# Optimization experiments

Measured on AMD Instinct MI355X. Metric: run time of the kernel, lower is better.

The kernel has to match this reference:

```python
import jax, jax.numpy as jnp
import numpy as np
from jax import lax

B, C, D, H, W = 4, 256, 32, 32, 32
LATENT = 512


def setup_inputs() -> dict:
    key = jax.random.key(0)
    k = jax.random.split(key, 6)
    x = jax.random.normal(k[0], (B, C, D, H, W), dtype=jnp.float32)
    prev_rgb = jax.random.normal(k[1], (B, 1, D, H, W), dtype=jnp.float32)
    istyle = jax.random.normal(k[2], (B, LATENT), dtype=jnp.float32)
    # nn.Linear(latent_dim, input_channel): weight [C, LATENT], bias [C]
    lim = 1.0 / np.sqrt(LATENT)
    W_style = jax.random.uniform(k[3], (C, LATENT), minval=-lim, maxval=lim, dtype=jnp.float32)
    b_style = jax.random.uniform(k[4], (C,), minval=-lim, maxval=lim, dtype=jnp.float32)
    # Conv3DMod weight [out=1, C, 1,1,1], kaiming_normal fan_in, leaky_relu(a=0) gain=sqrt(2)
    conv_weight = jax.random.normal(k[5], (1, C, 1, 1, 1), dtype=jnp.float32) * np.float32(np.sqrt(2.0 / C))
    return {"x": x, "prev_rgb": prev_rgb, "istyle": istyle,
            "W_style": W_style, "b_style": b_style, "conv_weight": conv_weight}


def _blur3d(x):
    # kornia filter3d with normalized 3x3x3 [1,2,1] outer-product kernel, replicate padding
    f = jnp.array([1.0, 2.0, 1.0], dtype=x.dtype)
    ker = f[:, None, None] * f[None, :, None] * f[None, None, :]
    ker = (ker / ker.sum())[None, None]  # [1,1,3,3,3] (single channel)
    xp = jnp.pad(x, ((0, 0), (0, 0), (1, 1), (1, 1), (1, 1)), mode='edge')
    return lax.conv_general_dilated(
        xp, ker, window_strides=(1, 1, 1), padding='VALID',
        dimension_numbers=('NCDHW', 'OIDHW', 'NCDHW'))


def reference(x, prev_rgb, istyle, W_style, b_style, conv_weight):
    b, c, d, h, w = x.shape
    # to_style linear
    style = istyle @ W_style.T + b_style                    # [b, c]
    # Conv3DMod, kernel=1, demod=False: per-sample modulated weights reduce to a
    # per-(sample, channel) coefficient; conv is a channel-weighted sum.
    wk = conv_weight[0, :, 0, 0, 0]                         # [c]
    coef = wk[None, :] * (style + 1.0)                      # [b, c]
    out = jnp.einsum('bcdhw,bc->bdhw', x, coef)[:, None]    # [b,1,d,h,w]
    out = out + prev_rgb
    # Upsample scale=2, trilinear, align_corners=False (half-pixel centers)
    out = jax.image.resize(out, (b, 1, 2 * d, 2 * h, 2 * w), method='trilinear')
    out = _blur3d(out)
    return out
```

## Files before the change

### kernel.cpp

```cpp
#include <hip/hip_runtime.h>

#define BATCH 4
#define CH    256
#define SVOL  32768
#define SV4   8192
#define NC    4
#define CCH   64


__global__ void __launch_bounds__(256)
coef_kernel(const float* __restrict__ istyle,
            const float* __restrict__ W_style,
            const float* __restrict__ b_style,
            const float* __restrict__ wk,
            float* __restrict__ coef) {
    int tid  = threadIdx.x;
    int wave = blockIdx.x * 4 + (tid >> 6);
    int lane = tid & 63;
    int b = wave >> 8;
    int c = wave & 255;
    const float* is = istyle + b * 512;
    const float* wr = W_style + c * 512;
    float acc = 0.f;
    #pragma unroll
    for (int j = 0; j < 8; ++j) {
        int k = lane + j * 64;
        acc += is[k] * wr[k];
    }
    #pragma unroll
    for (int off = 32; off >= 1; off >>= 1)
        acc += __shfl_down(acc, off, 64);
    if (lane == 0)
        coef[b * 256 + c] = wk[c] * (acc + b_style[c] + 1.0f);
}

__global__ void __launch_bounds__(256)
reduce_c_kernel(const float4* __restrict__ x4,
                const float* __restrict__ coef,
                float4* __restrict__ partial4) {
    __shared__ float cf[CCH];
    int chunk = blockIdx.y;
    int g  = blockIdx.x * 256 + threadIdx.x;
    int b  = g >> 13;
    int s4 = g & (SV4 - 1);
    if (threadIdx.x < CCH)
        cf[threadIdx.x] = coef[b * 256 + chunk * CCH + threadIdx.x];
    __syncthreads();
    const float4* xp = x4 + (size_t)(b * CH + chunk * CCH) * SV4 + s4;
    float4 acc = {0.f, 0.f, 0.f, 0.f};
    #pragma unroll 16
    for (int cc = 0; cc < CCH; ++cc) {
        float4 v = xp[(size_t)cc * SV4];
        float w = cf[cc];
        acc.x += v.x * w; acc.y += v.y * w;
        acc.z += v.z * w; acc.w += v.w * w;
    }
    partial4[(size_t)(chunk * BATCH + b) * SV4 + s4] = acc;
}

__global__ void __launch_bounds__(256)
finalize_small_kernel(const float4* __restrict__ partial4,
                      const float4* __restrict__ prev4,
                      float4* __restrict__ small4) {
    int g  = blockIdx.x * 256 + threadIdx.x;
    int b  = g >> 13;
    int s4 = g & (SV4 - 1);
    float4 acc = prev4[g];
    #pragma unroll
    for (int chunk = 0; chunk < NC; ++chunk) {
        float4 p = partial4[(size_t)(chunk * BATCH + b) * SV4 + s4];
        acc.x += p.x; acc.y += p.y; acc.z += p.z; acc.w += p.w;
    }
    small4[g] = acc;
}

__global__ void __launch_bounds__(256)
upblur_kernel(const float* __restrict__ small,
              float* __restrict__ out) {
    int g  = blockIdx.x * 256 + threadIdx.x;
    int xo = g & 63;
    int yo = (g >> 6) & 63;
    int zo = (g >> 12) & 63;
    int b  = g >> 18;

    int jx = xo >> 1, jy = yo >> 1, jz = zo >> 1;
    int px = xo & 1,  py = yo & 1,  pz = zo & 1;

    int xi[3] = { jx > 0 ? jx - 1 : 0, jx, jx < 31 ? jx + 1 : 31 };
    int yi[3] = { jy > 0 ? jy - 1 : 0, jy, jy < 31 ? jy + 1 : 31 };
    int zi[3] = { jz > 0 ? jz - 1 : 0, jz, jz < 31 ? jz + 1 : 31 };

    float wx[3] = { px ? 1.f : 5.f, 10.f, px ? 5.f : 1.f };
    float wy[3] = { py ? 1.f : 5.f, 10.f, py ? 5.f : 1.f };
    float wz[3] = { pz ? 1.f : 5.f, 10.f, pz ? 5.f : 1.f };

    const float* base = small + (size_t)b * SVOL;
    float acc = 0.f;
    #pragma unroll
    for (int a = 0; a < 3; ++a) {
        const float* pzrow = base + zi[a] * 1024;
        float accy = 0.f;
        #pragma unroll
        for (int c = 0; c < 3; ++c) {
            const float* pyrow = pzrow + yi[c] * 32;
            float row = wx[0] * pyrow[xi[0]] + wx[1] * pyrow[xi[1]] + wx[2] * pyrow[xi[2]];
            accy += wy[c] * row;
        }
        acc += wz[a] * accy;
    }
    out[g] = acc * (1.0f / 4096.0f);
}

extern "C" void kernel_launch(void* const* d_in, const int* in_sizes, int n_in,
                              void* d_out, int out_size, void* d_ws, size_t ws_size,
                              hipStream_t stream) {
    const float* x       = (const float*)d_in[0];
    const float* prev    = (const float*)d_in[1];
    const float* istyle  = (const float*)d_in[2];
    const float* W_style = (const float*)d_in[3];
    const float* b_style = (const float*)d_in[4];
    const float* wk      = (const float*)d_in[5];
    float* ws      = (float*)d_ws;
    float* coef    = ws;
    float* partial = ws + 1024;
    float* small   = partial + (size_t)NC * BATCH * SVOL;

    coef_kernel<<<256, 256, 0, stream>>>(istyle, W_style, b_style, wk, coef);

    dim3 g2(BATCH * SV4 / 256, NC);
    reduce_c_kernel<<<g2, 256, 0, stream>>>((const float4*)x, coef, (float4*)partial);

    finalize_small_kernel<<<BATCH * SV4 / 256, 256, 0, stream>>>(
        (const float4*)partial, (const float4*)prev, (float4*)small);

    upblur_kernel<<<BATCH * 64 * 64 * 64 / 256, 256, 0, stream>>>(small, (float*)d_out);
}
```

Baseline: 208.7 us.

## Fuse channel reduction and finalize via in-block LDS split-channel reduction

The channel-weighted reduction now splits the 256 channels across 8 wave groups inside one block, each covering 32 spatial float4 positions. Partial sums are combined in shared memory and prev_rgb is added in the same kernel. This removes the global partial buffer, its write and re-read, and one kernel launch. Loads of x also switch to nontemporal hints. Each wave now reads only 32 contiguous float4 per channel row (512B segments), and only one warp in eight does the final sum, which could affect memory coalescing efficiency.

```diff
diff --git a/kernel.cpp b/kernel.cpp
--- a/kernel.cpp
+++ b/kernel.cpp
@@ -4,8 +4,11 @@
 #define CH    256
 #define SVOL  32768
 #define SV4   8192
-#define NC    4
-#define CCH   64
+#define TILE  32
+#define NCH   8
+#define CCH   32
+
+typedef float floatx4 __attribute__((ext_vector_type(4)));
 
 
 __global__ void __launch_bounds__(256)
@@ -35,43 +38,41 @@
 }
 
 __global__ void __launch_bounds__(256)
-reduce_c_kernel(const float4* __restrict__ x4,
+reduce_c_kernel(const floatx4* __restrict__ x4,
                 const float* __restrict__ coef,
-                float4* __restrict__ partial4) {
-    __shared__ float cf[CCH];
-    int chunk = blockIdx.y;
-    int g  = blockIdx.x * 256 + threadIdx.x;
-    int b  = g >> 13;
-    int s4 = g & (SV4 - 1);
-    if (threadIdx.x < CCH)
-        cf[threadIdx.x] = coef[b * 256 + chunk * CCH + threadIdx.x];
+                const floatx4* __restrict__ prev4,
+                floatx4* __restrict__ small4) {
+    __shared__ float   cf[CH];
+    __shared__ floatx4 red[NCH][TILE];
+
+    int t     = threadIdx.x;
+    int pos   = t & (TILE - 1);
+    int chunk = t >> 5;
+    int gpos  = blockIdx.x * TILE + pos;
+    int b     = gpos >> 13;
+    int s4    = gpos & (SV4 - 1);
+
+    cf[t] = coef[b * CH + t];
     __syncthreads();
-    const float4* xp = x4 + (size_t)(b * CH + chunk * CCH) * SV4 + s4;
-    float4 acc = {0.f, 0.f, 0.f, 0.f};
+
+    const floatx4* xp = x4 + (size_t)(b * CH + chunk * CCH) * SV4 + s4;
+    floatx4 acc = {0.f, 0.f, 0.f, 0.f};
     #pragma unroll 16
     for (int cc = 0; cc < CCH; ++cc) {
-        float4 v = xp[(size_t)cc * SV4];
-        float w = cf[cc];
-        acc.x += v.x * w; acc.y += v.y * w;
-        acc.z += v.z * w; acc.w += v.w * w;
+        floatx4 v = __builtin_nontemporal_load(&xp[(size_t)cc * SV4]);
+        float   w = cf[chunk * CCH + cc];
+        acc += v * w;
     }
-    partial4[(size_t)(chunk * BATCH + b) * SV4 + s4] = acc;
-}
+    red[chunk][pos] = acc;
+    __syncthreads();
 
-__global__ void __launch_bounds__(256)
-finalize_small_kernel(const float4* __restrict__ partial4,
-                      const float4* __restrict__ prev4,
-                      float4* __restrict__ small4) {
-    int g  = blockIdx.x * 256 + threadIdx.x;
-    int b  = g >> 13;
-    int s4 = g & (SV4 - 1);
-    float4 acc = prev4[g];
-    #pragma unroll
-    for (int chunk = 0; chunk < NC; ++chunk) {
-        float4 p = partial4[(size_t)(chunk * BATCH + b) * SV4 + s4];
-        acc.x += p.x; acc.y += p.y; acc.z += p.z; acc.w += p.w;
+    if (t < TILE) {
+        floatx4 r = prev4[gpos];
+        #pragma unroll
+        for (int k = 0; k < NCH; ++k)
+            r += red[k][t];
+        small4[gpos] = r;
     }
-    small4[g] = acc;
 }
 
 __global__ void __launch_bounds__(256)
@@ -120,18 +121,14 @@
     const float* W_style = (const float*)d_in[3];
     const float* b_style = (const float*)d_in[4];
     const float* wk      = (const float*)d_in[5];
-    float* ws      = (float*)d_ws;
-    float* coef    = ws;
-    float* partial = ws + 1024;
-    float* small   = partial + (size_t)NC * BATCH * SVOL;
+    float* ws    = (float*)d_ws;
+    float* coef  = ws;
+    float* small = ws + 1024;
 
     coef_kernel<<<256, 256, 0, stream>>>(istyle, W_style, b_style, wk, coef);
 
-    dim3 g2(BATCH * SV4 / 256, NC);
-    reduce_c_kernel<<<g2, 256, 0, stream>>>((const float4*)x, coef, (float4*)partial);
-
-    finalize_small_kernel<<<BATCH * SV4 / 256, 256, 0, stream>>>(
-        (const float4*)partial, (const float4*)prev, (float4*)small);
+    reduce_c_kernel<<<BATCH * SV4 / TILE, 256, 0, stream>>>(
+        (const floatx4*)x, coef, (const floatx4*)prev, (floatx4*)small);
 
     upblur_kernel<<<BATCH * 64 * 64 * 64 / 256, 256, 0, stream>>>(small, (float*)d_out);
 }
```

Result: faster. 195.9 us (-6.1%).
